# Kernel optimization log

Measured on AMD Instinct MI355X. Metric: run time of the kernel, lower is better.

Reference implementation:

```python
import jax, jax.numpy as jnp
import numpy as np

N_INST = 100000
N_NET = 100000
E = 1600000
H = 64
OUT = 32
L = 2


def setup_inputs() -> dict:
    key = jax.random.key(0)
    ks = jax.random.split(key, 16)
    inp = {
        "x_inst": jax.random.normal(ks[0], (N_INST, H), jnp.float32),
        "x_net": jax.random.normal(ks[1], (N_NET, H), jnp.float32),
        "edge_i2n": jax.random.randint(ks[2], (2, E), 0, N_INST, jnp.int32),
        "edge_n2i": jax.random.randint(ks[3], (2, E), 0, N_NET, jnp.int32),
        # stacked GAT params: axis0 = layer, axis1 = relation (0: inst->net, 1: net->inst)
        "W_src": jax.random.normal(ks[4], (L, 2, H, H), jnp.float32) * 0.1,
        "W_dst": jax.random.normal(ks[5], (L, 2, H, H), jnp.float32) * 0.1,
        "att_src": jax.random.normal(ks[6], (L, 2, H), jnp.float32) * 0.1,
        "att_dst": jax.random.normal(ks[7], (L, 2, H), jnp.float32) * 0.1,
        "bias_g": jax.random.normal(ks[8], (L, 2, H), jnp.float32) * 0.1,
        "lin1_w": jax.random.normal(ks[9], (H, OUT), jnp.float32) * 0.1,
        "lin1_b": jax.random.normal(ks[10], (OUT,), jnp.float32) * 0.1,
        "lin2_w": jax.random.normal(ks[11], (OUT, 1), jnp.float32) * 0.1,
        "lin2_b": jax.random.normal(ks[12], (1,), jnp.float32) * 0.1,
    }
    return inp


def _segment_softmax(scores, seg, n_seg):
    # numerically stable softmax over edges grouped by destination node
    m = jax.ops.segment_max(scores, seg, num_segments=n_seg)
    e = jnp.exp(scores - m[seg])
    s = jax.ops.segment_sum(e, seg, num_segments=n_seg)
    return e / (s[seg] + 1e-16)


def _gat_conv(x_src, x_dst, edge, Ws, Wd, a_s, a_d, b, n_dst):
    # PyG GATConv, heads=1, add_self_loops=False, eval mode (dropout inactive)
    hs = x_src @ Ws  # [Ns, H]
    hd = x_dst @ Wd  # [Nd, H]
    src, dst = edge[0], edge[1]
    score = (hs * a_s).sum(-1)[src] + (hd * a_d).sum(-1)[dst]  # [E]
    alpha = _segment_softmax(jax.nn.leaky_relu(score, 0.2), dst, n_dst)
    out = jax.ops.segment_sum(hs[src] * alpha[:, None], dst, num_segments=n_dst)
    return out + b


def reference(x_inst, x_net, edge_i2n, edge_n2i, W_src, W_dst, att_src, att_dst,
              bias_g, lin1_w, lin1_b, lin2_w, lin2_b):
    xi, xn = x_inst, x_net
    for l in range(L):
        new_net = _gat_conv(xi, xn, edge_i2n, W_src[l, 0], W_dst[l, 0],
                            att_src[l, 0], att_dst[l, 0], bias_g[l, 0], xn.shape[0])
        new_inst = _gat_conv(xn, xi, edge_n2i, W_src[l, 1], W_dst[l, 1],
                             att_src[l, 1], att_dst[l, 1], bias_g[l, 1], xi.shape[0])
        xn = jax.nn.relu(new_net)
        xi = jax.nn.relu(new_inst)
    h = jax.nn.relu(xn @ lin1_w + lin1_b)
    return h @ lin2_w + lin2_b  # [N_net, 1]
```

## Files before the change

kernel.cpp:

```cpp
#include <hip/hip_runtime.h>
#include <hip/hip_fp16.h>

#define H 64
#define BSHIFT 9
#define BUCKET 512
#define NBMAX 256
#define CHUNK 4096
#define PREF 16
#define PREF2 16

__device__ __forceinline__ int bcasti(int x, int j) {
    return __builtin_amdgcn_readlane(x, j);
}
__device__ __forceinline__ float bcastf(float x, int j) {
    return __uint_as_float((unsigned)__builtin_amdgcn_readlane((int)__float_as_uint(x), j));
}

__global__ void wvec3_kernel(const float* __restrict__ W_dst, const float* __restrict__ att_dst,
                             float* __restrict__ v2all) {
    int b = blockIdx.x;
    int k = threadIdx.x;
    const float* Wd = W_dst + (size_t)b * H * H;
    const float* ad = att_dst + (size_t)b * H;
    float s2 = 0.f;
    for (int j = 0; j < H; ++j) s2 += Wd[k * H + j] * ad[j];
    v2all[b * H + k] = s2;
}

__device__ __forceinline__ void proj_body(float* __restrict__ Wl, int blk,
                                          const float* __restrict__ x, const float* __restrict__ W,
                                          const float* __restrict__ as_, const float* __restrict__ v2d,
                                          __half* __restrict__ hs, float* __restrict__ ssrc,
                                          float* __restrict__ sdst_out, int n) {
    int t = threadIdx.x;
    for (int i = t; i < H * H; i += 256) Wl[i] = W[i];
    __syncthreads();
    int lane = t & 63;
    int w = t >> 6;
    int row0 = blk * 16 + w * 4;
    if (row0 >= n) return;
    int rem = n - row0;
    float asl = as_[lane];
    const float* xp = x + (size_t)row0 * H + lane;
    float xr0 = xp[0];
    float xr1 = rem > 1 ? xp[H] : 0.f;
    float xr2 = rem > 2 ? xp[2 * H] : 0.f;
    float xr3 = rem > 3 ? xp[3 * H] : 0.f;
    float a0 = 0.f, a1 = 0.f, a2 = 0.f, a3 = 0.f;
#pragma unroll
    for (int k = 0; k < H; ++k) {
        float wv = Wl[k * H + lane];
        a0 = fmaf(bcastf(xr0, k), wv, a0);
        a1 = fmaf(bcastf(xr1, k), wv, a1);
        a2 = fmaf(bcastf(xr2, k), wv, a2);
        a3 = fmaf(bcastf(xr3, k), wv, a3);
    }
    __half* hp = hs + (size_t)row0 * H + lane;
    hp[0] = __float2half_rn(a0);
    if (rem > 1) hp[H] = __float2half_rn(a1);
    if (rem > 2) hp[2 * H] = __float2half_rn(a2);
    if (rem > 3) hp[3 * H] = __float2half_rn(a3);
    float p0 = a0 * asl, p1 = a1 * asl, p2 = a2 * asl, p3 = a3 * asl;
#pragma unroll
    for (int off = 32; off; off >>= 1) {
        p0 += __shfl_xor(p0, off); p1 += __shfl_xor(p1, off);
        p2 += __shfl_xor(p2, off); p3 += __shfl_xor(p3, off);
    }
    if (lane == 0) {
        ssrc[row0] = p0;
        if (rem > 1) ssrc[row0 + 1] = p1;
        if (rem > 2) ssrc[row0 + 2] = p2;
        if (rem > 3) ssrc[row0 + 3] = p3;
    }
    if (sdst_out) {
        float vl = v2d[lane];
        float q0 = xr0 * vl, q1 = xr1 * vl, q2 = xr2 * vl, q3 = xr3 * vl;
#pragma unroll
        for (int off = 32; off; off >>= 1) {
            q0 += __shfl_xor(q0, off); q1 += __shfl_xor(q1, off);
            q2 += __shfl_xor(q2, off); q3 += __shfl_xor(q3, off);
        }
        if (lane == 0) {
            sdst_out[row0] = q0;
            if (rem > 1) sdst_out[row0 + 1] = q1;
            if (rem > 2) sdst_out[row0 + 2] = q2;
            if (rem > 3) sdst_out[row0 + 3] = q3;
        }
    }
}

__global__ void hist_proj_kernel(const int* __restrict__ dstA, const int* __restrict__ dstB,
                                 int* __restrict__ cntA, int* __restrict__ cntB,
                                 int ne, int nch, int nbA, int nbB,
                                 const float* __restrict__ x, const float* __restrict__ W,
                                 const float* __restrict__ as_, const float* __restrict__ v2d,
                                 __half* __restrict__ hs, float* __restrict__ ssrc,
                                 float* __restrict__ sdst_out, int n) {
    __shared__ float smem[H * H];
    int blk = blockIdx.x;
    if (blk < 2 * nch) {
        int* h = (int*)smem;
        bool second = blk >= nch;
        const int* dst = second ? dstB : dstA;
        int* cnt = second ? cntB : cntA;
        int nb = second ? nbB : nbA;
        int c = second ? blk - nch : blk;
        int beg = c * CHUNK, end = beg + CHUNK;
        if (end > ne) end = ne;
        int t = threadIdx.x;
        for (int i = t; i < NBMAX; i += 256) h[i] = 0;
        __syncthreads();
        for (int i = beg + t; i < end; i += 256) atomicAdd(&h[dst[i] >> BSHIFT], 1);
        __syncthreads();
        for (int b = t; b < nb; b += 256) cnt[(size_t)b * nch + c] = h[b];
        return;
    }
    proj_body(smem, blk - 2 * nch, x, W, as_, v2d, hs, ssrc, sdst_out, n);
}

__global__ void scan_chunks(int* __restrict__ cntA, int* __restrict__ cntB,
                            int* __restrict__ totA, int* __restrict__ totB,
                            int nch, int nbA) {
    __shared__ int sm[512];
    int b = blockIdx.x;
    bool second = b >= nbA;
    int* cnt = second ? cntB : cntA;
    int* tot = second ? totB : totA;
    if (second) b -= nbA;
    int t = threadIdx.x;
    int v = t < nch ? cnt[(size_t)b * nch + t] : 0;
    sm[t] = v;
    __syncthreads();
    for (int off = 1; off < 512; off <<= 1) {
        int u = t >= off ? sm[t - off] : 0;
        __syncthreads();
        sm[t] += u;
        __syncthreads();
    }
    if (t < nch) cnt[(size_t)b * nch + t] = sm[t] - v;
    if (t == 511) tot[b] = sm[511];
}

__global__ void scan_buckets(const int* __restrict__ totA, const int* __restrict__ totB,
                             int* __restrict__ bstartA, int* __restrict__ bstartB,
                             int nbA, int nbB, int ne) {
    __shared__ int sm[256];
    const int* tot = blockIdx.x ? totB : totA;
    int* bstart = blockIdx.x ? bstartB : bstartA;
    int nb = blockIdx.x ? nbB : nbA;
    int t = threadIdx.x;
    int v = t < nb ? tot[t] : 0;
    sm[t] = v;
    __syncthreads();
    for (int off = 1; off < 256; off <<= 1) {
        int u = t >= off ? sm[t - off] : 0;
        __syncthreads();
        sm[t] += u;
        __syncthreads();
    }
    if (t < nb) bstart[t] = sm[t] - v;
    if (t == 0) bstart[nb] = ne;
}

__global__ void scatter_proj_kernel(const int* __restrict__ srcA, const int* __restrict__ dstA,
                                    const int* __restrict__ cntA, const int* __restrict__ bstartA,
                                    unsigned* __restrict__ tmpA,
                                    const int* __restrict__ srcB, const int* __restrict__ dstB,
                                    const int* __restrict__ cntB, const int* __restrict__ bstartB,
                                    unsigned* __restrict__ tmpB,
                                    int ne, int nch, int nbA, int nbB,
                                    const float* __restrict__ x, const float* __restrict__ W,
                                    const float* __restrict__ as_, const float* __restrict__ v2d,
                                    __half* __restrict__ hs, float* __restrict__ ssrc,
                                    float* __restrict__ sdst_out, int n) {
    __shared__ float smem[H * H];
    int blk = blockIdx.x;
    if (blk < 2 * nch) {
        int* cur = (int*)smem;
        bool second = blk >= nch;
        const int* src = second ? srcB : srcA;
        const int* dst = second ? dstB : dstA;
        const int* cnt = second ? cntB : cntA;
        const int* bstart = second ? bstartB : bstartA;
        unsigned* tmp = second ? tmpB : tmpA;
        int nb = second ? nbB : nbA;
        int c = second ? blk - nch : blk;
        int beg = c * CHUNK, end = beg + CHUNK;
        if (end > ne) end = ne;
        int t = threadIdx.x;
        for (int b = t; b < nb; b += 256) cur[b] = bstart[b] + cnt[(size_t)b * nch + c];
        __syncthreads();
        for (int i = beg + t; i < end; i += 256) {
            int d = dst[i];
            int pos = atomicAdd(&cur[d >> BSHIFT], 1);
            unsigned rec = ((unsigned)(d & (BUCKET - 1)) << 17) | (unsigned)src[i];
            tmp[pos] = rec;
        }
        return;
    }
    proj_body(smem, blk - 2 * nch, x, W, as_, v2d, hs, ssrc, sdst_out, n);
}

__global__ void proj_kernel(const float* __restrict__ x, const float* __restrict__ W,
                            const float* __restrict__ as_, const float* __restrict__ v2d,
                            __half* __restrict__ hs, float* __restrict__ ssrc,
                            float* __restrict__ sdst_out, int n) {
    __shared__ float smem[H * H];
    proj_body(smem, blockIdx.x, x, W, as_, v2d, hs, ssrc, sdst_out, n);
}

__global__ void bucket_finalize(const unsigned* __restrict__ tmpA, const int* __restrict__ bstartA,
                                int* __restrict__ rowptrA, int* __restrict__ srcsA,
                                int ndstA, int nbA,
                                const unsigned* __restrict__ tmpB, const int* __restrict__ bstartB,
                                int* __restrict__ rowptrB, int* __restrict__ srcsB,
                                int ndstB) {
    __shared__ int cnt[BUCKET];
    __shared__ int sm[BUCKET];
    __shared__ int cur[BUCKET];
    int b = blockIdx.x;
    bool second = b >= nbA;
    const unsigned* tmp = second ? tmpB : tmpA;
    const int* bstart = second ? bstartB : bstartA;
    int* rowptr = second ? rowptrB : rowptrA;
    int* srcs   = second ? srcsB : srcsA;
    int ndst    = second ? ndstB : ndstA;
    if (second) b -= nbA;

    int t = threadIdx.x;
    int base = bstart[b], endi = bstart[b + 1];
    cnt[t] = 0;
    __syncthreads();
    for (int i = base + t; i < endi; i += 512)
        atomicAdd(&cnt[tmp[i] >> 17], 1);
    __syncthreads();
    int c0 = cnt[t];
    sm[t] = c0;
    __syncthreads();
    for (int off = 1; off < 512; off <<= 1) {
        int u = t >= off ? sm[t - off] : 0;
        __syncthreads();
        sm[t] += u;
        __syncthreads();
    }
    int d0 = b << BSHIFT;
    int e = base + sm[t] - c0;
    cur[t] = e;
    if (d0 + t < ndst) rowptr[d0 + t] = e;
    if (t == 0) {
        int hi = d0 + BUCKET;
        if (hi > ndst) hi = ndst;
        rowptr[hi] = endi;
    }
    __syncthreads();
    for (int i = base + t; i < endi; i += 512) {
        unsigned rec = tmp[i];
        int pos = atomicAdd(&cur[rec >> 17], 1);
        srcs[pos] = (int)(rec & 0x1FFFFu);
    }
}

__device__ __forceinline__ float gat_aggregate(const int* __restrict__ rowptr,
                                               const int* __restrict__ srcs,
                                               const float* __restrict__ ssrc,
                                               float sdst,
                                               const __half* __restrict__ hs,
                                               const float* __restrict__ bias,
                                               int wid, int lane) {
    int beg = rowptr[wid], end = rowptr[wid + 1];
    int cnt = end - beg;
    float acc0 = 0.f, acc1 = 0.f, acc2 = 0.f, acc3 = 0.f;
    float acc4 = 0.f, acc5 = 0.f, acc6 = 0.f, acc7 = 0.f;
    float l;

    if (cnt <= 64) {
        bool valid = lane < cnt;
        int s_l = valid ? srcs[beg + lane] : 0;
        float ss = valid ? ssrc[s_l] : 0.f;

        const __half* hsl = hs + lane;
        __half hv[PREF];
#pragma unroll
        for (int k = 0; k < PREF; ++k) {
            hv[k] = hsl[(size_t)bcasti(s_l, k) * H];
        }

        float sc = ss + sdst;
        sc = sc > 0.f ? sc : 0.2f * sc;
        float ev_l = valid ? __expf(sc) : 0.f;
        float ll = ev_l;
#pragma unroll
        for (int off = 32; off; off >>= 1) ll += __shfl_xor(ll, off);
        l = ll;

        bool more = cnt > PREF;
        __half hv2[PREF2];
        if (more) {
#pragma unroll
            for (int k = 0; k < PREF2; ++k) {
                hv2[k] = hsl[(size_t)bcasti(s_l, PREF + k) * H];
            }
        }

#pragma unroll
        for (int k = 0; k < PREF; k += 8) {
            acc0 += bcastf(ev_l, k + 0) * __half2float(hv[k + 0]);
            acc1 += bcastf(ev_l, k + 1) * __half2float(hv[k + 1]);
            acc2 += bcastf(ev_l, k + 2) * __half2float(hv[k + 2]);
            acc3 += bcastf(ev_l, k + 3) * __half2float(hv[k + 3]);
            acc4 += bcastf(ev_l, k + 4) * __half2float(hv[k + 4]);
            acc5 += bcastf(ev_l, k + 5) * __half2float(hv[k + 5]);
            acc6 += bcastf(ev_l, k + 6) * __half2float(hv[k + 6]);
            acc7 += bcastf(ev_l, k + 7) * __half2float(hv[k + 7]);
        }
        if (more) {
#pragma unroll
            for (int k = 0; k < PREF2; k += 8) {
                acc0 += bcastf(ev_l, PREF + k + 0) * __half2float(hv2[k + 0]);
                acc1 += bcastf(ev_l, PREF + k + 1) * __half2float(hv2[k + 1]);
                acc2 += bcastf(ev_l, PREF + k + 2) * __half2float(hv2[k + 2]);
                acc3 += bcastf(ev_l, PREF + k + 3) * __half2float(hv2[k + 3]);
                acc4 += bcastf(ev_l, PREF + k + 4) * __half2float(hv2[k + 4]);
                acc5 += bcastf(ev_l, PREF + k + 5) * __half2float(hv2[k + 5]);
                acc6 += bcastf(ev_l, PREF + k + 6) * __half2float(hv2[k + 6]);
                acc7 += bcastf(ev_l, PREF + k + 7) * __half2float(hv2[k + 7]);
            }
            int j = PREF + PREF2;
            for (; j + 3 < cnt; j += 4) {
                acc0 += bcastf(ev_l, j + 0) * __half2float(hsl[(size_t)bcasti(s_l, j + 0) * H]);
                acc1 += bcastf(ev_l, j + 1) * __half2float(hsl[(size_t)bcasti(s_l, j + 1) * H]);
                acc2 += bcastf(ev_l, j + 2) * __half2float(hsl[(size_t)bcasti(s_l, j + 2) * H]);
                acc3 += bcastf(ev_l, j + 3) * __half2float(hsl[(size_t)bcasti(s_l, j + 3) * H]);
            }
            for (; j < cnt; ++j)
                acc0 += bcastf(ev_l, j) * __half2float(hsl[(size_t)bcasti(s_l, j) * H]);
        }
    } else {
        const __half* hsl = hs + lane;
        float mm = -3.4e38f;
        for (int base = beg; base < end; base += 64) {
            int idx = base + lane;
            if (idx < end) {
                float sc = ssrc[srcs[idx]] + sdst;
                sc = sc > 0.f ? sc : 0.2f * sc;
                mm = fmaxf(mm, sc);
            }
        }
#pragma unroll
        for (int off = 32; off; off >>= 1) mm = fmaxf(mm, __shfl_xor(mm, off));
        float ll = 0.f;
        for (int base = beg; base < end; base += 64) {
            int idx = base + lane;
            int c2 = end - base; if (c2 > 64) c2 = 64;
            int s_l = idx < end ? srcs[idx] : 0;
            float ev_l = 0.f;
            if (idx < end) {
                float sc = ssrc[s_l] + sdst;
                sc = sc > 0.f ? sc : 0.2f * sc;
                ev_l = __expf(sc - mm);
            }
            ll += ev_l;
            int j = 0;
            for (; j + 1 < c2; j += 2) {
                acc0 += bcastf(ev_l, j) * __half2float(hsl[(size_t)bcasti(s_l, j) * H]);
                acc1 += bcastf(ev_l, j + 1) * __half2float(hsl[(size_t)bcasti(s_l, j + 1) * H]);
            }
            if (j < c2)
                acc0 += bcastf(ev_l, j) * __half2float(hsl[(size_t)bcasti(s_l, j) * H]);
        }
#pragma unroll
        for (int off = 32; off; off >>= 1) ll += __shfl_xor(ll, off);
        l = ll;
    }
    float v = ((acc0 + acc1) + (acc2 + acc3)) + ((acc4 + acc5) + (acc6 + acc7));
    v = v / (l + 1e-16f) + bias[lane];
    return v > 0.f ? v : 0.f;
}

__global__ void gat01_kernel(const int* __restrict__ rp0, const int* __restrict__ sr0,
                             const float* __restrict__ ssrc0, const float* __restrict__ sdst0,
                             const __half* __restrict__ hs0, const float* __restrict__ bias0,
                             const float* __restrict__ v2next, float* __restrict__ sdstNext, int n0,
                             const int* __restrict__ rp1, const int* __restrict__ sr1,
                             const float* __restrict__ ssrc1, const float* __restrict__ sdst1,
                             const __half* __restrict__ hs1, const float* __restrict__ bias1,
                             float* __restrict__ out1, int n1) {
    int nblk0 = (n0 + 3) / 4;
    int lane = threadIdx.x & 63;
    if ((int)blockIdx.x < nblk0) {
        int wid = (int)((blockIdx.x * blockDim.x + threadIdx.x) >> 6);
        if (wid >= n0) return;
        float v = gat_aggregate(rp0, sr0, ssrc0, sdst0[wid], hs0, bias0, wid, lane);
        float q = v * v2next[lane];
#pragma unroll
        for (int off = 32; off; off >>= 1) q += __shfl_xor(q, off);
        if (lane == 0) sdstNext[wid] = q;
    } else {
        int wid = (int)(((blockIdx.x - nblk0) * blockDim.x + threadIdx.x) >> 6);
        if (wid >= n1) return;
        float v = gat_aggregate(rp1, sr1, ssrc1, sdst1[wid], hs1, bias1, wid, lane);
        out1[(size_t)wid * H + lane] = v;
    }
}

__global__ void gat_node_mlp_kernel(const int* __restrict__ rowptr, const int* __restrict__ srcs,
                                    const float* __restrict__ ssrc, const float* __restrict__ sdstArr,
                                    const __half* __restrict__ hs, const float* __restrict__ bias,
                                    const float* __restrict__ w1, const float* __restrict__ b1,
                                    const float* __restrict__ w2, const float* __restrict__ b2,
                                    float* __restrict__ out, int ndst) {
    __shared__ float W1[H * 32];
    __shared__ float W2[32];
    __shared__ float B1[32];
    {
        int t = threadIdx.x;
        for (int i = t; i < H * 32; i += 256) W1[i] = w1[i];
        if (t < 32) { W2[t] = w2[t]; B1[t] = b1[t]; }
        __syncthreads();
    }
    int wid = (int)((blockIdx.x * blockDim.x + threadIdx.x) >> 6);
    int lane = threadIdx.x & 63;
    if (wid >= ndst) return;
    float v = gat_aggregate(rowptr, srcs, ssrc, sdstArr[wid], hs, bias, wid, lane);

    int c = lane & 31;
    int kbase = (lane >> 5) << 5;
    float s = 0.f;
#pragma unroll
    for (int k = 0; k < 32; ++k) s += __shfl(v, kbase + k) * W1[(kbase + k) * 32 + c];
    s += __shfl_xor(s, 32);
    s += B1[c];
    s = s > 0.f ? s : 0.f;
    float q = s * W2[c];
#pragma unroll
    for (int off = 16; off; off >>= 1) q += __shfl_xor(q, off);
    if (lane == 0) out[wid] = q + b2[0];
}

extern "C" void kernel_launch(void* const* d_in, const int* in_sizes, int n_in,
                              void* d_out, int out_size, void* d_ws, size_t ws_size,
                              hipStream_t stream) {
    const float* x_inst  = (const float*)d_in[0];
    const float* x_net   = (const float*)d_in[1];
    const int*   e_i2n   = (const int*)d_in[2];
    const int*   e_n2i   = (const int*)d_in[3];
    const float* W_src   = (const float*)d_in[4];
    const float* W_dst   = (const float*)d_in[5];
    const float* att_src = (const float*)d_in[6];
    const float* att_dst = (const float*)d_in[7];
    const float* bias_g  = (const float*)d_in[8];
    const float* lin1_w  = (const float*)d_in[9];
    const float* lin1_b  = (const float*)d_in[10];
    const float* lin2_w  = (const float*)d_in[11];
    const float* lin2_b  = (const float*)d_in[12];

    const int n_inst = in_sizes[0] / H;
    const int n_net  = in_sizes[1] / H;
    const int ne     = in_sizes[2] / 2;
    const int nmax   = n_inst > n_net ? n_inst : n_net;

    const int nbA = (n_net + BUCKET - 1) >> BSHIFT;
    const int nbB = (n_inst + BUCKET - 1) >> BSHIFT;
    const int nch = (ne + CHUNK - 1) / CHUNK;

    float* ws = (float*)d_ws;
    size_t off = 0;
    auto alloc = [&](size_t nelem) {
        off = (off + 3) & ~(size_t)3;
        float* p = ws + off; off += nelem; return p;
    };
    float* xiA     = alloc((size_t)n_inst * H);
    __half* hs0    = (__half*)alloc((size_t)nmax * H / 2);
    __half* hs1    = (__half*)alloc((size_t)nmax * H / 2);
    float* ssrc0   = alloc(nmax);
    float* ssrc1   = alloc(nmax);
    float* sdstA   = alloc(nmax);
    float* sdstB   = alloc(nmax);
    float* sdstC   = alloc(nmax);
    int*   rp_i2n  = (int*)alloc(nmax + 1);
    int*   sr_i2n  = (int*)alloc(ne);
    int*   rp_n2i  = (int*)alloc(nmax + 1);
    int*   sr_n2i  = (int*)alloc(ne);
    unsigned* tmpA = (unsigned*)alloc(ne);
    unsigned* tmpB = (unsigned*)alloc(ne);
    int*   cntA    = (int*)alloc((size_t)NBMAX * nch);
    int*   cntB    = (int*)alloc((size_t)NBMAX * nch);
    int*   totA    = (int*)alloc(NBMAX);
    int*   totB    = (int*)alloc(NBMAX);
    int*   bstartA = (int*)alloc(NBMAX + 1);
    int*   bstartB = (int*)alloc(NBMAX + 1);
    float* v2all   = alloc(3 * H);
    (void)ws_size;

    const int* dstA = e_i2n + ne;
    const int* dstB = e_n2i + ne;

    wvec3_kernel<<<3, 64, 0, stream>>>(W_dst, att_dst, v2all);

    {
        int grid = 2 * nch + (n_inst + 15) / 16;
        hist_proj_kernel<<<grid, 256, 0, stream>>>(dstA, dstB, cntA, cntB, ne, nch, nbA, nbB,
                                                   x_inst, W_src + 0 * H * H, att_src + 0 * H,
                                                   v2all + 1 * H, hs0, ssrc0, sdstB, n_inst);
    }
    scan_chunks<<<nbA + nbB, 512, 0, stream>>>(cntA, cntB, totA, totB, nch, nbA);
    scan_buckets<<<2, 256, 0, stream>>>(totA, totB, bstartA, bstartB, nbA, nbB, ne);
    {
        int grid = 2 * nch + (n_net + 15) / 16;
        scatter_proj_kernel<<<grid, 256, 0, stream>>>(e_i2n, dstA, cntA, bstartA, tmpA,
                                                      e_n2i, dstB, cntB, bstartB, tmpB,
                                                      ne, nch, nbA, nbB,
                                                      x_net, W_src + 1 * H * H, att_src + 1 * H,
                                                      v2all + 0 * H, hs1, ssrc1, sdstA, n_net);
    }
    bucket_finalize<<<nbA + nbB, 512, 0, stream>>>(tmpA, bstartA, rp_i2n, sr_i2n, n_net, nbA,
                                                   tmpB, bstartB, rp_n2i, sr_n2i, n_inst);

    {
        int grid = (n_net + 3) / 4 + (n_inst + 3) / 4;
        gat01_kernel<<<grid, 256, 0, stream>>>(rp_i2n, sr_i2n, ssrc0, sdstA, hs0, bias_g + 0 * H,
                                               v2all + 2 * H, sdstC, n_net,
                                               rp_n2i, sr_n2i, ssrc1, sdstB, hs1, bias_g + 1 * H,
                                               xiA, n_inst);
    }
    proj_kernel<<<(n_inst + 15) / 16, 256, 0, stream>>>(xiA, W_src + 2 * H * H, att_src + 2 * H,
                                                        nullptr, hs0, ssrc0, nullptr, n_inst);
    gat_node_mlp_kernel<<<(n_net + 3) / 4, 256, 0, stream>>>(rp_i2n, sr_i2n, ssrc0, sdstC,
                                                             hs0, bias_g + 2 * H,
                                                             lin1_w, lin1_b, lin2_w, lin2_b,
                                                             (float*)d_out, n_net);
}
```

Measured before the change: 329.5 us.

## Fuse layer-2 source projection into GAT aggregation kernel, simplify prefetch

The layer-2 inst-side projection (x @ W_src and the attention source score) now runs inside gat01_kernel's second branch on each freshly aggregated row. This removes the xiA fp32 intermediate and the separate proj_kernel launch. Every block in that branch now loads a 16KB weight tile into shared memory, so LDS use rises for the whole kernel. Results go to new hs2/ssrc2 buffers, and the aggregation prefetch becomes a single 32-element stage in place of two 16-element stages.

```diff
diff --git a/kernel.cpp b/kernel.cpp
--- a/kernel.cpp
+++ b/kernel.cpp
@@ -6,8 +6,7 @@
 #define BUCKET 512
 #define NBMAX 256
 #define CHUNK 4096
-#define PREF 16
-#define PREF2 16
+#define PREF 32
 
 __device__ __forceinline__ int bcasti(int x, int j) {
     return __builtin_amdgcn_readlane(x, j);
@@ -201,14 +200,6 @@
     proj_body(smem, blk - 2 * nch, x, W, as_, v2d, hs, ssrc, sdst_out, n);
 }
 
-__global__ void proj_kernel(const float* __restrict__ x, const float* __restrict__ W,
-                            const float* __restrict__ as_, const float* __restrict__ v2d,
-                            __half* __restrict__ hs, float* __restrict__ ssrc,
-                            float* __restrict__ sdst_out, int n) {
-    __shared__ float smem[H * H];
-    proj_body(smem, blockIdx.x, x, W, as_, v2d, hs, ssrc, sdst_out, n);
-}
-
 __global__ void bucket_finalize(const unsigned* __restrict__ tmpA, const int* __restrict__ bstartA,
                                 int* __restrict__ rowptrA, int* __restrict__ srcsA,
                                 int ndstA, int nbA,
@@ -293,15 +284,6 @@
         for (int off = 32; off; off >>= 1) ll += __shfl_xor(ll, off);
         l = ll;
 
-        bool more = cnt > PREF;
-        __half hv2[PREF2];
-        if (more) {
-#pragma unroll
-            for (int k = 0; k < PREF2; ++k) {
-                hv2[k] = hsl[(size_t)bcasti(s_l, PREF + k) * H];
-            }
-        }
-
 #pragma unroll
         for (int k = 0; k < PREF; k += 8) {
             acc0 += bcastf(ev_l, k + 0) * __half2float(hv[k + 0]);
@@ -313,28 +295,15 @@
             acc6 += bcastf(ev_l, k + 6) * __half2float(hv[k + 6]);
             acc7 += bcastf(ev_l, k + 7) * __half2float(hv[k + 7]);
         }
-        if (more) {
-#pragma unroll
-            for (int k = 0; k < PREF2; k += 8) {
-                acc0 += bcastf(ev_l, PREF + k + 0) * __half2float(hv2[k + 0]);
-                acc1 += bcastf(ev_l, PREF + k + 1) * __half2float(hv2[k + 1]);
-                acc2 += bcastf(ev_l, PREF + k + 2) * __half2float(hv2[k + 2]);
-                acc3 += bcastf(ev_l, PREF + k + 3) * __half2float(hv2[k + 3]);
-                acc4 += bcastf(ev_l, PREF + k + 4) * __half2float(hv2[k + 4]);
-                acc5 += bcastf(ev_l, PREF + k + 5) * __half2float(hv2[k + 5]);
-                acc6 += bcastf(ev_l, PREF + k + 6) * __half2float(hv2[k + 6]);
-                acc7 += bcastf(ev_l, PREF + k + 7) * __half2float(hv2[k + 7]);
-            }
-            int j = PREF + PREF2;
-            for (; j + 3 < cnt; j += 4) {
-                acc0 += bcastf(ev_l, j + 0) * __half2float(hsl[(size_t)bcasti(s_l, j + 0) * H]);
-                acc1 += bcastf(ev_l, j + 1) * __half2float(hsl[(size_t)bcasti(s_l, j + 1) * H]);
-                acc2 += bcastf(ev_l, j + 2) * __half2float(hsl[(size_t)bcasti(s_l, j + 2) * H]);
-                acc3 += bcastf(ev_l, j + 3) * __half2float(hsl[(size_t)bcasti(s_l, j + 3) * H]);
-            }
-            for (; j < cnt; ++j)
-                acc0 += bcastf(ev_l, j) * __half2float(hsl[(size_t)bcasti(s_l, j) * H]);
-        }
+        int j = PREF;
+        for (; j + 3 < cnt; j += 4) {
+            acc0 += bcastf(ev_l, j + 0) * __half2float(hsl[(size_t)bcasti(s_l, j + 0) * H]);
+            acc1 += bcastf(ev_l, j + 1) * __half2float(hsl[(size_t)bcasti(s_l, j + 1) * H]);
+            acc2 += bcastf(ev_l, j + 2) * __half2float(hsl[(size_t)bcasti(s_l, j + 2) * H]);
+            acc3 += bcastf(ev_l, j + 3) * __half2float(hsl[(size_t)bcasti(s_l, j + 3) * H]);
+        }
+        for (; j < cnt; ++j)
+            acc0 += bcastf(ev_l, j) * __half2float(hsl[(size_t)bcasti(s_l, j) * H]);
     } else {
         const __half* hsl = hs + lane;
         float mm = -3.4e38f;
@@ -384,7 +353,9 @@
                              const int* __restrict__ rp1, const int* __restrict__ sr1,
                              const float* __restrict__ ssrc1, const float* __restrict__ sdst1,
                              const __half* __restrict__ hs1, const float* __restrict__ bias1,
-                             float* __restrict__ out1, int n1) {
+                             const float* __restrict__ Wsrc2, const float* __restrict__ as2,
+                             __half* __restrict__ hs2, float* __restrict__ ssrc2, int n1) {
+    __shared__ float Wl[H * H];
     int nblk0 = (n0 + 3) / 4;
     int lane = threadIdx.x & 63;
     if ((int)blockIdx.x < nblk0) {
@@ -396,10 +367,20 @@
         for (int off = 32; off; off >>= 1) q += __shfl_xor(q, off);
         if (lane == 0) sdstNext[wid] = q;
     } else {
+        int t = threadIdx.x;
+        for (int i = t; i < H * H; i += 256) Wl[i] = Wsrc2[i];
+        __syncthreads();
         int wid = (int)(((blockIdx.x - nblk0) * blockDim.x + threadIdx.x) >> 6);
         if (wid >= n1) return;
         float v = gat_aggregate(rp1, sr1, ssrc1, sdst1[wid], hs1, bias1, wid, lane);
-        out1[(size_t)wid * H + lane] = v;
+        float a = 0.f;
+#pragma unroll
+        for (int k = 0; k < H; ++k) a = fmaf(bcastf(v, k), Wl[k * H + lane], a);
+        hs2[(size_t)wid * H + lane] = __float2half_rn(a);
+        float p = a * as2[lane];
+#pragma unroll
+        for (int off = 32; off; off >>= 1) p += __shfl_xor(p, off);
+        if (lane == 0) ssrc2[wid] = p;
     }
 }
 
@@ -469,11 +450,12 @@
         off = (off + 3) & ~(size_t)3;
         float* p = ws + off; off += nelem; return p;
     };
-    float* xiA     = alloc((size_t)n_inst * H);
     __half* hs0    = (__half*)alloc((size_t)nmax * H / 2);
     __half* hs1    = (__half*)alloc((size_t)nmax * H / 2);
+    __half* hs2    = (__half*)alloc((size_t)nmax * H / 2);
     float* ssrc0   = alloc(nmax);
     float* ssrc1   = alloc(nmax);
+    float* ssrc2   = alloc(nmax);
     float* sdstA   = alloc(nmax);
     float* sdstB   = alloc(nmax);
     float* sdstC   = alloc(nmax);
@@ -521,12 +503,11 @@
         gat01_kernel<<<grid, 256, 0, stream>>>(rp_i2n, sr_i2n, ssrc0, sdstA, hs0, bias_g + 0 * H,
                                                v2all + 2 * H, sdstC, n_net,
                                                rp_n2i, sr_n2i, ssrc1, sdstB, hs1, bias_g + 1 * H,
-                                               xiA, n_inst);
-    }
-    proj_kernel<<<(n_inst + 15) / 16, 256, 0, stream>>>(xiA, W_src + 2 * H * H, att_src + 2 * H,
-                                                        nullptr, hs0, ssrc0, nullptr, n_inst);
-    gat_node_mlp_kernel<<<(n_net + 3) / 4, 256, 0, stream>>>(rp_i2n, sr_i2n, ssrc0, sdstC,
-                                                             hs0, bias_g + 2 * H,
+                                               W_src + 2 * H * H, att_src + 2 * H,
+                                               hs2, ssrc2, n_inst);
+    }
+    gat_node_mlp_kernel<<<(n_net + 3) / 4, 256, 0, stream>>>(rp_i2n, sr_i2n, ssrc2, sdstC,
+                                                             hs2, bias_g + 2 * H,
                                                              lin1_w, lin1_b, lin2_w, lin2_b,
                                                              (float*)d_out, n_net);
 }
```

After: 331.6 us. About the same (+0.6%).
